# Performance work log

Measured on AMD Instinct MI355X. Metric: run time of the kernel, lower is better.

## Reference

```python
import jax, jax.numpy as jnp
import numpy as np

N = 20000      # nodes
E = 320000     # edges
IN = 300       # input_channel
HID = 100      # hidden_channel (= heads*out_channels with heads=1)
R = 50         # num_relations
B = 8          # num_bases (the 4th positional arg 'heads'=8 lands on num_bases in PyG RGATConv)
HEADS = 1
CLS = 3
Q = 64         # number of query (aspect) nodes
EPS = 1e-16


def setup_inputs() -> dict:
    key = jax.random.key(0)
    ks = jax.random.split(key, 16)
    x = jax.random.normal(ks[0], (N, IN), jnp.float32)
    edge_index = jax.random.randint(ks[1], (2, E), 0, N)
    edge_type = jax.random.randint(ks[2], (E,), 0, R)
    query_indices = jax.random.randint(ks[3], (Q,), 0, N)

    def w(k, shape, scale):
        return jax.random.normal(k, shape, jnp.float32) * scale

    comp1 = w(ks[4], (R, B), 0.3)
    basis1 = w(ks[5], (B, IN, HEADS * HID), 1.0 / np.sqrt(IN))
    q1 = w(ks[6], (HEADS * HID, HEADS), 0.1)
    k1 = w(ks[7], (HEADS * HID, HEADS), 0.1)
    b1 = jnp.zeros((HEADS * HID,), jnp.float32)
    comp2 = w(ks[8], (R, B), 0.3)
    basis2 = w(ks[9], (B, HID, HEADS * HID), 1.0 / np.sqrt(HID))
    q2 = w(ks[10], (HEADS * HID, HEADS), 0.1)
    k2 = w(ks[11], (HEADS * HID, HEADS), 0.1)
    b2 = jnp.zeros((HEADS * HID,), jnp.float32)
    Wl = w(ks[12], (CLS, HID), 1.0 / np.sqrt(HID))
    bl = jnp.zeros((CLS,), jnp.float32)
    return dict(x=x, edge_index=edge_index, edge_type=edge_type,
                query_indices=query_indices,
                comp1=comp1, basis1=basis1, q1=q1, k1=k1, b1=b1,
                comp2=comp2, basis2=basis2, q2=q2, k2=k2, b2=b2,
                Wl=Wl, bl=bl)


def segment_softmax(alpha, seg, num_segments):
    # numerically-stable softmax over edges grouped by destination node
    m = jax.ops.segment_max(alpha, seg, num_segments=num_segments)  # [N, H]
    e = jnp.exp(alpha - m[seg])
    s = jax.ops.segment_sum(e, seg, num_segments=num_segments)
    return e / (s[seg] + EPS)


def rgat_conv(x, edge_index, edge_type, comp, basis, q, k, b):
    # basis-decomposed per-relation weight: [R, in, H*out]
    W = jnp.einsum('rb,bio->rio', comp, basis)
    # transform every node under every relation once, then gather per edge
    xt = jnp.einsum('ni,rio->nro', x, W)          # [N, R, H*out]
    src, dst = edge_index[0], edge_index[1]        # j -> i (source_to_target)
    xi = xt[dst, edge_type]                        # [E, H*out]
    xj = xt[src, edge_type]                        # [E, H*out]
    qi = xi @ q                                    # [E, H]
    kj = xj @ k                                    # [E, H]
    alpha = jax.nn.leaky_relu(qi + kj, 0.2)        # additive self-attention
    alpha = segment_softmax(alpha, dst, N)         # across-relation softmax
    msg = xj.reshape(E, HEADS, HID) * alpha[:, :, None]
    out = jax.ops.segment_sum(msg, dst, num_segments=N)  # [N, H, out]
    return out.reshape(N, HEADS * HID) + b         # concat=True


def reference(x, edge_index, edge_type, query_indices,
              comp1, basis1, q1, k1, b1,
              comp2, basis2, q2, k2, b2, Wl, bl):
    h = jax.nn.relu(rgat_conv(x, edge_index, edge_type, comp1, basis1, q1, k1, b1))
    h = jax.nn.relu(rgat_conv(h, edge_index, edge_type, comp2, basis2, q2, k2, b2))
    pooled = h[query_indices].mean(axis=0)          # [HID]
    return pooled @ Wl.T + bl                       # [CLS]
```

## Files before the change

kernel.cpp:

```cpp
#include <hip/hip_runtime.h>
#include <math.h>

#define N_NODES 20000
#define E_EDGES 320000
#define IN_CH   300
#define HID     100
#define R_REL   50
#define NB      8
#define CLS     3
#define NQ      64
#define OUTW    800
#define ZW      128
#define KP1     320
#define KP2     128
#define SCAN_BLKS ((N_NODES + 255) / 256)

typedef unsigned short ushort_t;
typedef __attribute__((ext_vector_type(8))) short     short8;
typedef __attribute__((ext_vector_type(8))) unsigned short ushort8;
typedef __attribute__((ext_vector_type(4))) float     f32x4;
typedef __attribute__((ext_vector_type(2))) float     f32x2;

__device__ __forceinline__ ushort_t f2bf_rne(float f) {
    unsigned u = __float_as_uint(f);
    unsigned r = (u + 0x7fffu + ((u >> 16) & 1u)) >> 16;
    return (ushort_t)r;
}
__device__ __forceinline__ float bf2f(ushort_t u) {
    return __uint_as_float((unsigned)u << 16);
}

__global__ __launch_bounds__(256) void zero_deg2(int* __restrict__ dd,
                                                 int* __restrict__ ds) {
    int i = blockIdx.x * 256 + threadIdx.x;
    if (i < N_NODES) { dd[i] = 0; ds[i] = 0; }
}

__global__ __launch_bounds__(256) void hist2_kernel(
        const int* __restrict__ ei, int* __restrict__ dd,
        int* __restrict__ ds) {
    int e = blockIdx.x * 256 + threadIdx.x;
    if (e < E_EDGES) {
        atomicAdd(&dd[ei[E_EDGES + e]], 1);
        atomicAdd(&ds[ei[e]], 1);
    }
}

__global__ __launch_bounds__(256) void scan1_both(
        const int* __restrict__ deg_d, int* __restrict__ rp_d, int* __restrict__ bsum_d,
        const int* __restrict__ deg_s, int* __restrict__ rp_s, int* __restrict__ bsum_s) {
    int set = blockIdx.x / SCAN_BLKS, blk = blockIdx.x % SCAN_BLKS;
    const int* deg = set ? deg_s : deg_d;
    int* rowptr    = set ? rp_s  : rp_d;
    int* bsum      = set ? bsum_s : bsum_d;
    __shared__ int s[256];
    int tid = threadIdx.x;
    int idx = blk * 256 + tid;
    int v = (idx < N_NODES) ? deg[idx] : 0;
    s[tid] = v; __syncthreads();
    #pragma unroll
    for (int off = 1; off < 256; off <<= 1) {
        int t = (tid >= off) ? s[tid - off] : 0;
        __syncthreads();
        s[tid] += t;
        __syncthreads();
    }
    if (idx < N_NODES) rowptr[idx] = s[tid] - v;
    if (tid == 255) bsum[blk] = s[255];
}

__global__ __launch_bounds__(128) void scan2_both(
        int* __restrict__ bsum_d, int* __restrict__ rp_d,
        int* __restrict__ bsum_s, int* __restrict__ rp_s) {
    int* bsum   = blockIdx.x ? bsum_s : bsum_d;
    int* rowptr = blockIdx.x ? rp_s   : rp_d;
    __shared__ int s[128];
    int tid = threadIdx.x;
    int v = (tid < SCAN_BLKS) ? bsum[tid] : 0;
    s[tid] = v; __syncthreads();
    #pragma unroll
    for (int off = 1; off < 128; off <<= 1) {
        int t = (tid >= off) ? s[tid - off] : 0;
        __syncthreads();
        s[tid] += t;
        __syncthreads();
    }
    if (tid < SCAN_BLKS) bsum[tid] = s[tid] - v;
    if (tid == 0) rowptr[N_NODES] = E_EDGES;
}

__global__ __launch_bounds__(256) void scan3_both(
        int* __restrict__ rp_d, const int* __restrict__ bsum_d, int* __restrict__ cur_d,
        int* __restrict__ rp_s, const int* __restrict__ bsum_s, int* __restrict__ cur_s) {
    int set = blockIdx.x / SCAN_BLKS, blk = blockIdx.x % SCAN_BLKS;
    int* rowptr      = set ? rp_s   : rp_d;
    const int* bsum  = set ? bsum_s : bsum_d;
    int* cursor      = set ? cur_s  : cur_d;
    int idx = blk * 256 + threadIdx.x;
    if (idx < N_NODES) {
        int v = rowptr[idx] + bsum[blk];
        rowptr[idx] = v;
        cursor[idx] = v;
    }
}

__global__ __launch_bounds__(256) void scatter_both(
        const int* __restrict__ ei, const int* __restrict__ et,
        int* __restrict__ cur_d, int* __restrict__ cur_s,
        int* __restrict__ skey, int* __restrict__ skey_s,
        int* __restrict__ zidx) {
    int e = blockIdx.x * 256 + threadIdx.x;
    if (e >= E_EDGES) return;
    int s = ei[e], d = ei[E_EDGES + e], rt = et[e];
    int p = atomicAdd(&cur_d[d], 1);
    skey[p] = (s << 6) | rt;
    int qp = atomicAdd(&cur_s[s], 1);
    skey_s[qp] = rt;
    zidx[p] = qp;
}

__global__ __launch_bounds__(256) void split_bt_both(
        const float* __restrict__ basis1, ushort_t* __restrict__ Bt1,
        const float* __restrict__ basis2, ushort_t* __restrict__ Bt2) {
    int idx = blockIdx.x * 256 + threadIdx.x;
    const int n1 = OUTW * KP1;
    if (idx < n1) {
        int n = idx / KP1, k = idx - n * KP1;
        int b = n / HID, o = n - b * HID;
        float v = (k < IN_CH) ? basis1[((size_t)b * IN_CH + k) * HID + o] : 0.f;
        Bt1[idx] = f2bf_rne(v);
    } else {
        int i2 = idx - n1;
        if (i2 >= OUTW * KP2) return;
        int n = i2 / KP2, k = i2 - n * KP2;
        int b = n / HID, o = n - b * HID;
        float v = (k < HID) ? basis2[((size_t)b * HID + k) * HID + o] : 0.f;
        Bt2[i2] = f2bf_rne(v);
    }
}

#define BM 16
#define BN 160
#define NCB (OUTW / BN)
__global__ __launch_bounds__(128) void gemm_mfma(
        const float* __restrict__ A, const ushort_t* __restrict__ Bt,
        ushort_t* __restrict__ xbh, int M, int K, int Kp, int do_relu) {
    __shared__ ushort_t As[BM * 328];
    __shared__ ushort_t Bs[BN * 32];
    int tid  = threadIdx.x;
    int lane = tid & 63, wave = tid >> 6;
    int ml = lane & 15, quad = lane >> 4;
    int wc = wave * 80;
    int row0 = blockIdx.x * BM;
    int SW = Kp + 8;
    int ksteps = Kp >> 5;

    {
        int ra = tid >> 3;
        int gr = row0 + ra;
        const float* ar = A + (size_t)gr * K;
        for (int c = (tid & 7); c * 8 < Kp; c += 8) {
            int kb = c * 8;
            float vals[8];
            if (gr < M) {
                if (kb + 8 <= K) {
                    float4 f0 = *(const float4*)&ar[kb];
                    float4 f1 = *(const float4*)&ar[kb + 4];
                    vals[0]=f0.x; vals[1]=f0.y; vals[2]=f0.z; vals[3]=f0.w;
                    vals[4]=f1.x; vals[5]=f1.y; vals[6]=f1.z; vals[7]=f1.w;
                } else {
                    #pragma unroll
                    for (int i = 0; i < 8; i++)
                        vals[i] = (kb + i < K) ? ar[kb + i] : 0.f;
                }
                if (do_relu)
                    #pragma unroll
                    for (int i = 0; i < 8; i++) vals[i] = fmaxf(vals[i], 0.f);
            } else {
                #pragma unroll
                for (int i = 0; i < 8; i++) vals[i] = 0.f;
            }
            ushort8 hv;
            #pragma unroll
            for (int i = 0; i < 8; i++) hv[i] = f2bf_rne(vals[i]);
            *(ushort8*)&As[ra * SW + kb] = hv;
        }
    }

    for (int cb = 0; cb < NCB; cb++) {
        int col0 = cb * BN;
        f32x4 acc[5] = {};
        for (int ks = 0; ks < ksteps; ks++) {
            int k0 = ks << 5;
            __syncthreads();
            for (int t = tid; t < 640; t += 128) {
                int rb = t >> 2, ch = t & 3;
                __builtin_amdgcn_global_load_lds(
                    (const __attribute__((address_space(1))) unsigned int*)
                        &Bt[(size_t)(col0 + rb) * Kp + k0 + ch * 8],
                    (__attribute__((address_space(3))) unsigned int*)&Bs[t * 8],
                    16, 0, 0);
            }
            __syncthreads();
            short8 af, bf[5];
            af = *(const short8*)&As[ml * SW + k0 + quad * 8];
            #pragma unroll
            for (int nt = 0; nt < 5; nt++)
                bf[nt] = *(const short8*)&Bs[(wc + nt * 16 + ml) * 32 + quad * 8];
            #pragma unroll
            for (int nt = 0; nt < 5; nt++)
                acc[nt] = __builtin_amdgcn_mfma_f32_16x16x32_bf16(af, bf[nt], acc[nt], 0, 0, 0);
        }
        #pragma unroll
        for (int nt = 0; nt < 5; nt++) {
            #pragma unroll
            for (int r = 0; r < 4; r++) {
                int grow = row0 + quad * 4 + r;
                if (grow < M)
                    xbh[(size_t)grow * OUTW + col0 + wc + nt * 16 + ml] =
                        f2bf_rne(acc[nt][r]);
            }
        }
    }
}

__global__ __launch_bounds__(256) void qk3_kernel(
        const ushort_t* __restrict__ xbh, const float* __restrict__ q,
        const float* __restrict__ k, float* __restrict__ xbq,
        float* __restrict__ xbk) {
    __shared__ float sq[HID], sk[HID];
    int tid = threadIdx.x;
    if (tid < HID) { sq[tid] = q[tid]; sk[tid] = k[tid]; }
    __syncthreads();
    int idx = blockIdx.x * 256 + tid;
    if (idx >= N_NODES * NB) return;
    const ushort_t* xr = xbh + (size_t)(idx >> 3) * OUTW + (idx & 7) * HID;
    float aq = 0.f, ak = 0.f;
    #pragma unroll
    for (int c = 0; c < 25; c++) {
        ushort4 v = *(const ushort4*)&xr[c * 4];
        #pragma unroll
        for (int i = 0; i < 4; i++) {
            float f = bf2f(((const ushort_t*)&v)[i]);
            aq = fmaf(f, sq[c * 4 + i], aq);
            ak = fmaf(f, sk[c * 4 + i], ak);
        }
    }
    xbq[idx] = aq;
    xbk[idx] = ak;
}

__global__ __launch_bounds__(256) void compute_z(
        const int* __restrict__ rowptr_s, const int* __restrict__ skey_s,
        const float* __restrict__ comp, const ushort_t* __restrict__ xbh,
        ushort_t* __restrict__ Z) {
    __shared__ float scomp[R_REL * NB];
    int tid = threadIdx.x;
    for (int i = tid; i < R_REL * NB; i += 256) scomp[i] = comp[i];
    __syncthreads();
    int wave = tid >> 6, lane = tid & 63;
    int s = blockIdx.x * 4 + wave;
    if (s >= N_NODES) return;
    int beg = rowptr_s[s], end = rowptr_s[s + 1];
    if (beg == end) return;
    int eg = lane >> 4, c16 = lane & 15;
    int cbase = c16 * 8;
    float xr[NB][8];
    #pragma unroll
    for (int b = 0; b < NB; b++)
        #pragma unroll
        for (int i = 0; i < 8; i++) xr[b][i] = 0.f;
    if (cbase < HID) {
        #pragma unroll
        for (int b = 0; b < NB; b++) {
            const ushort_t* base = xbh + (size_t)s * OUTW + b * HID + cbase;
            ushort4 v0 = *(const ushort4*)base;
            xr[b][0] = bf2f(v0.x); xr[b][1] = bf2f(v0.y);
            xr[b][2] = bf2f(v0.z); xr[b][3] = bf2f(v0.w);
            if (cbase + 8 <= HID) {
                ushort4 v1 = *(const ushort4*)(base + 4);
                xr[b][4] = bf2f(v1.x); xr[b][5] = bf2f(v1.y);
                xr[b][6] = bf2f(v1.z); xr[b][7] = bf2f(v1.w);
            }
        }
    }
    for (int w0 = beg; w0 < end; w0 += 64) {
        int kw = (w0 + lane < end) ? skey_s[w0 + lane] : 0;
        int wend = w0 + 64 < end ? w0 + 64 : end;
        for (int p0 = w0; p0 < wend; p0 += 4) {
            int j = p0 - w0 + eg;
            int rt = __shfl(kw, j) & 63;
            int p = p0 + eg;
            const float* cr = &scomp[rt * NB];
            float z[8] = {};
            #pragma unroll
            for (int b = 0; b < NB; b++) {
                float cb = cr[b];
                #pragma unroll
                for (int i = 0; i < 8; i++) z[i] = fmaf(cb, xr[b][i], z[i]);
            }
            ushort8 zz;
            #pragma unroll
            for (int i = 0; i < 8; i++) zz[i] = f2bf_rne(z[i]);
            if (p < end)
                *(ushort8*)&Z[(size_t)p * ZW + cbase] = zz;
        }
    }
}

__global__ __launch_bounds__(256) void msg_soft(
        const int* __restrict__ rowptr, const int* __restrict__ skey,
        const int* __restrict__ zidx,
        const float* __restrict__ comp, const ushort_t* __restrict__ Z,
        const float* __restrict__ xbq, const float* __restrict__ xbk,
        const float* __restrict__ bias, float* __restrict__ h) {
    __shared__ float scomp[R_REL * NB];
    int tid = threadIdx.x;
    for (int i = tid; i < R_REL * NB; i += 256) scomp[i] = comp[i];
    __syncthreads();
    int wave = tid >> 6, lane = tid & 63;
    int d = blockIdx.x * 4 + wave;
    if (d >= N_NODES) return;
    int beg = rowptr[d], end = rowptr[d + 1];

    float4 qd0 = *(const float4*)&xbq[d * NB];
    float4 qd1 = *(const float4*)&xbq[d * NB + 4];

    int l5 = lane & 31;
    bool act = l5 < 25;
    int oc = l5 * 4;
    f32x4 acc = {0.f, 0.f, 0.f, 0.f};
    float m = -1e30f, l = 0.f;

    for (int c0 = beg; c0 < end; c0 += 64) {
        int p = c0 + lane;
        bool valid = p < end;
        float a = -1e30f;
        int zi = 0;
        if (valid) {
            int key = skey[p];
            zi = zidx[p];
            int s = key >> 6, rt = key & 63;
            const float4 c0v = *(const float4*)&scomp[rt * NB];
            const float4 c1v = *(const float4*)&scomp[rt * NB + 4];
            const float4 k0v = *(const float4*)&xbk[s * NB];
            const float4 k1v = *(const float4*)&xbk[s * NB + 4];
            float qi = c0v.x*qd0.x + c0v.y*qd0.y + c0v.z*qd0.z + c0v.w*qd0.w
                     + c1v.x*qd1.x + c1v.y*qd1.y + c1v.z*qd1.z + c1v.w*qd1.w;
            float kj = c0v.x*k0v.x + c0v.y*k0v.y + c0v.z*k0v.z + c0v.w*k0v.w
                     + c1v.x*k1v.x + c1v.y*k1v.y + c1v.z*k1v.z + c1v.w*k1v.w;
            a = qi + kj;
            a = a > 0.f ? a : 0.2f * a;
        }
        float cm = a;
        #pragma unroll
        for (int off = 32; off; off >>= 1) cm = fmaxf(cm, __shfl_xor(cm, off));
        float M = fmaxf(m, cm);
        float scale = __expf(m - M);
        acc *= scale; l *= scale; m = M;
        float wgt = valid ? __expf(a - M) : 0.f;
        float cs = wgt;
        #pragma unroll
        for (int off = 32; off; off >>= 1) cs += __shfl_xor(cs, off);
        l += cs;
        int cnt = end - c0; if (cnt > 64) cnt = 64;
        for (int j = 0; j < cnt; j += 2) {
            int jj = j + (lane >> 5);
            float wj = __shfl(wgt, jj);
            int   zj = __shfl(zi, jj);
            if (act) {
                ushort4 zz = *(const ushort4*)&Z[(size_t)zj * ZW + oc];
                acc.x = fmaf(wj, bf2f(zz.x), acc.x);
                acc.y = fmaf(wj, bf2f(zz.y), acc.y);
                acc.z = fmaf(wj, bf2f(zz.z), acc.z);
                acc.w = fmaf(wj, bf2f(zz.w), acc.w);
            }
        }
    }
    #pragma unroll
    for (int i = 0; i < 4; i++) acc[i] += __shfl_xor(acc[i], 32);
    if (lane < 25) {
        float inv = 1.f / (l + 1e-16f);
        float4 r;
        r.x = bias[oc]     + acc.x * inv;
        r.y = bias[oc + 1] + acc.y * inv;
        r.z = bias[oc + 2] + acc.z * inv;
        r.w = bias[oc + 3] + acc.w * inv;
        *(float4*)&h[(size_t)d * HID + oc] = r;
    }
}

__global__ __launch_bounds__(128) void head_kernel(
        const float* __restrict__ h2, const int* __restrict__ qidx,
        const float* __restrict__ Wl, const float* __restrict__ bl,
        float* __restrict__ out) {
    __shared__ float pooled[HID];
    int tid = threadIdx.x;
    if (tid < HID) {
        float s = 0.f;
        for (int i = 0; i < NQ; i++)
            s += fmaxf(h2[(size_t)qidx[i] * HID + tid], 0.f);
        pooled[tid] = s * (1.0f / NQ);
    }
    __syncthreads();
    if (tid < CLS) {
        float s = bl[tid];
        for (int o = 0; o < HID; o++) s = fmaf(pooled[o], Wl[tid * HID + o], s);
        out[tid] = s;
    }
}

extern "C" void kernel_launch(void* const* d_in, const int* in_sizes, int n_in,
                              void* d_out, int out_size, void* d_ws, size_t ws_size,
                              hipStream_t stream) {
    const float* x      = (const float*)d_in[0];
    const int*   ei     = (const int*)  d_in[1];
    const int*   et     = (const int*)  d_in[2];
    const int*   qidx   = (const int*)  d_in[3];
    const float* comp1  = (const float*)d_in[4];
    const float* basis1 = (const float*)d_in[5];
    const float* q1     = (const float*)d_in[6];
    const float* k1     = (const float*)d_in[7];
    const float* b1     = (const float*)d_in[8];
    const float* comp2  = (const float*)d_in[9];
    const float* basis2 = (const float*)d_in[10];
    const float* q2     = (const float*)d_in[11];
    const float* k2     = (const float*)d_in[12];
    const float* b2     = (const float*)d_in[13];
    const float* Wl     = (const float*)d_in[14];
    const float* bl     = (const float*)d_in[15];
    float* out = (float*)d_out;

    char* w = (char*)d_ws;
    size_t off = 0;
    auto alloc = [&](size_t nbytes) {
        void* p = (void*)(w + off);
        off += ((nbytes + 255) / 256) * 256;
        return p;
    };
    ushort_t* xbh    = (ushort_t*)alloc((size_t)N_NODES * OUTW * 2);
    ushort_t* Z      = (ushort_t*)alloc((size_t)E_EDGES * ZW * 2);
    float*    h1     = (float*)alloc((size_t)N_NODES * HID * 4);
    float*    h2     = (float*)alloc((size_t)N_NODES * HID * 4);
    ushort_t* Bt1    = (ushort_t*)alloc((size_t)OUTW * KP1 * 2);
    ushort_t* Bt2    = (ushort_t*)alloc((size_t)OUTW * KP2 * 2);
    float*    xbq    = (float*)alloc((size_t)N_NODES * NB * 4);
    float*    xbk    = (float*)alloc((size_t)N_NODES * NB * 4);
    int*      deg_d  = (int*)alloc(N_NODES * 4);
    int*      deg_s  = (int*)alloc(N_NODES * 4);
    int*      rp_d   = (int*)alloc((N_NODES + 1) * 4);
    int*      rp_s   = (int*)alloc((N_NODES + 1) * 4);
    int*      cur_d  = (int*)alloc(N_NODES * 4);
    int*      cur_s  = (int*)alloc(N_NODES * 4);
    int*      bsum_d = (int*)alloc(SCAN_BLKS * 4);
    int*      bsum_s = (int*)alloc(SCAN_BLKS * 4);
    int*      skey   = (int*)alloc(E_EDGES * 4);
    int*      skey_s = (int*)alloc(E_EDGES * 4);
    int*      zidx   = (int*)alloc(E_EDGES * 4);

    zero_deg2<<<SCAN_BLKS, 256, 0, stream>>>(deg_d, deg_s);
    hist2_kernel<<<(E_EDGES + 255) / 256, 256, 0, stream>>>(ei, deg_d, deg_s);
    scan1_both<<<2 * SCAN_BLKS, 256, 0, stream>>>(deg_d, rp_d, bsum_d, deg_s, rp_s, bsum_s);
    scan2_both<<<2, 128, 0, stream>>>(bsum_d, rp_d, bsum_s, rp_s);
    scan3_both<<<2 * SCAN_BLKS, 256, 0, stream>>>(rp_d, bsum_d, cur_d, rp_s, bsum_s, cur_s);
    scatter_both<<<(E_EDGES + 255) / 256, 256, 0, stream>>>(ei, et, cur_d, cur_s, skey, skey_s, zidx);
    split_bt_both<<<(OUTW * (KP1 + KP2) + 255) / 256, 256, 0, stream>>>(basis1, Bt1, basis2, Bt2);

    auto layer = [&](const float* input, int K, int Kp, int relu_in,
                     const ushort_t* Bt, const float* comp, const float* q,
                     const float* k, const float* bias, float* hout) {
        gemm_mfma<<<(N_NODES + BM - 1) / BM, 128, 0, stream>>>(input, Bt, xbh, N_NODES, K, Kp, relu_in);
        qk3_kernel<<<(N_NODES * NB + 255) / 256, 256, 0, stream>>>(xbh, q, k, xbq, xbk);
        compute_z<<<(N_NODES + 3) / 4, 256, 0, stream>>>(rp_s, skey_s, comp, xbh, Z);
        msg_soft<<<(N_NODES + 3) / 4, 256, 0, stream>>>(rp_d, skey, zidx, comp, Z, xbq, xbk, bias, hout);
    };

    layer(x,  IN_CH, KP1, 0, Bt1, comp1, q1, k1, b1, h1);
    layer(h1, HID,   KP2, 1, Bt2, comp2, q2, k2, b2, h2);
    head_kernel<<<1, 128, 0, stream>>>(h2, qidx, Wl, bl, out);
}
```

Measured before the change: 369.5 us.

## Restructure basis GEMM to register-held A fragments and direct global B loads

The basis GEMM is rewritten so each wave keeps its entire row of A as bf16 MFMA fragments in registers, and B fragments are read straight from global/L2 instead of being staged through LDS with per-k-step barriers. Blocks grow to 512 threads covering 64 rows by 160 columns per pass, and K and the ReLU flag become template parameters so the k-loop fully unrolls. This removes the LDS staging and the __syncthreads in the inner loop. In exchange it costs more registers (up to 10 A fragments), and each wave now fetches its B fragments from global/L2 on its own, since there is no cross-wave sharing through LDS.

```diff
diff --git a/kernel.cpp b/kernel.cpp
--- a/kernel.cpp
+++ b/kernel.cpp
@@ -139,77 +139,62 @@
     }
 }
 
-#define BM 16
-#define BN 160
-#define NCB (OUTW / BN)
-__global__ __launch_bounds__(128) void gemm_mfma(
+template<int K, int RELU>
+__global__ __launch_bounds__(512, 4) void gemm_mfma(
         const float* __restrict__ A, const ushort_t* __restrict__ Bt,
-        ushort_t* __restrict__ xbh, int M, int K, int Kp, int do_relu) {
-    __shared__ ushort_t As[BM * 328];
-    __shared__ ushort_t Bs[BN * 32];
+        ushort_t* __restrict__ xbh, int M) {
+    constexpr int KSTEPS = (K + 31) / 32;
+    constexpr int KP = KSTEPS * 32;
     int tid  = threadIdx.x;
     int lane = tid & 63, wave = tid >> 6;
+    int wr = wave >> 1, wc = wave & 1;
     int ml = lane & 15, quad = lane >> 4;
-    int wc = wave * 80;
-    int row0 = blockIdx.x * BM;
-    int SW = Kp + 8;
-    int ksteps = Kp >> 5;
-
+    int row0 = blockIdx.x * 64 + wr * 16;
+
+    short8 afrag[KSTEPS];
     {
-        int ra = tid >> 3;
-        int gr = row0 + ra;
+        int gr = row0 + ml;
+        bool rowok = gr < M;
         const float* ar = A + (size_t)gr * K;
-        for (int c = (tid & 7); c * 8 < Kp; c += 8) {
-            int kb = c * 8;
-            float vals[8];
-            if (gr < M) {
-                if (kb + 8 <= K) {
-                    float4 f0 = *(const float4*)&ar[kb];
-                    float4 f1 = *(const float4*)&ar[kb + 4];
-                    vals[0]=f0.x; vals[1]=f0.y; vals[2]=f0.z; vals[3]=f0.w;
-                    vals[4]=f1.x; vals[5]=f1.y; vals[6]=f1.z; vals[7]=f1.w;
-                } else {
-                    #pragma unroll
-                    for (int i = 0; i < 8; i++)
-                        vals[i] = (kb + i < K) ? ar[kb + i] : 0.f;
-                }
-                if (do_relu)
-                    #pragma unroll
-                    for (int i = 0; i < 8; i++) vals[i] = fmaxf(vals[i], 0.f);
+        #pragma unroll
+        for (int ks = 0; ks < KSTEPS; ks++) {
+            int kb = ks * 32 + quad * 8;
+            float v[8];
+            if (rowok && kb + 8 <= K) {
+                float4 f0 = *(const float4*)&ar[kb];
+                float4 f1 = *(const float4*)&ar[kb + 4];
+                v[0]=f0.x; v[1]=f0.y; v[2]=f0.z; v[3]=f0.w;
+                v[4]=f1.x; v[5]=f1.y; v[6]=f1.z; v[7]=f1.w;
             } else {
                 #pragma unroll
-                for (int i = 0; i < 8; i++) vals[i] = 0.f;
-            }
-            ushort8 hv;
-            #pragma unroll
-            for (int i = 0; i < 8; i++) hv[i] = f2bf_rne(vals[i]);
-            *(ushort8*)&As[ra * SW + kb] = hv;
-        }
-    }
-
-    for (int cb = 0; cb < NCB; cb++) {
-        int col0 = cb * BN;
+                for (int i = 0; i < 8; i++)
+                    v[i] = (rowok && kb + i < K) ? ar[kb + i] : 0.f;
+            }
+            if (RELU) {
+                #pragma unroll
+                for (int i = 0; i < 8; i++) v[i] = fmaxf(v[i], 0.f);
+            }
+            short8 hv;
+            #pragma unroll
+            for (int i = 0; i < 8; i++) hv[i] = (short)f2bf_rne(v[i]);
+            afrag[ks] = hv;
+        }
+    }
+
+    for (int cb = 0; cb < 5; cb++) {
+        int col0 = cb * 160 + wc * 80;
+        const ushort_t* bp0 = Bt + (size_t)(col0 + ml) * KP + quad * 8;
         f32x4 acc[5] = {};
-        for (int ks = 0; ks < ksteps; ks++) {
-            int k0 = ks << 5;
-            __syncthreads();
-            for (int t = tid; t < 640; t += 128) {
-                int rb = t >> 2, ch = t & 3;
-                __builtin_amdgcn_global_load_lds(
-                    (const __attribute__((address_space(1))) unsigned int*)
-                        &Bt[(size_t)(col0 + rb) * Kp + k0 + ch * 8],
-                    (__attribute__((address_space(3))) unsigned int*)&Bs[t * 8],
-                    16, 0, 0);
-            }
-            __syncthreads();
-            short8 af, bf[5];
-            af = *(const short8*)&As[ml * SW + k0 + quad * 8];
+        #pragma unroll
+        for (int ks = 0; ks < KSTEPS; ks++) {
+            short8 bf[5];
             #pragma unroll
             for (int nt = 0; nt < 5; nt++)
-                bf[nt] = *(const short8*)&Bs[(wc + nt * 16 + ml) * 32 + quad * 8];
+                bf[nt] = *(const short8*)(bp0 + (size_t)nt * 16 * KP + ks * 32);
             #pragma unroll
             for (int nt = 0; nt < 5; nt++)
-                acc[nt] = __builtin_amdgcn_mfma_f32_16x16x32_bf16(af, bf[nt], acc[nt], 0, 0, 0);
+                acc[nt] = __builtin_amdgcn_mfma_f32_16x16x32_bf16(
+                              afrag[ks], bf[nt], acc[nt], 0, 0, 0);
         }
         #pragma unroll
         for (int nt = 0; nt < 5; nt++) {
@@ -217,7 +202,7 @@
             for (int r = 0; r < 4; r++) {
                 int grow = row0 + quad * 4 + r;
                 if (grow < M)
-                    xbh[(size_t)grow * OUTW + col0 + wc + nt * 16 + ml] =
+                    xbh[(size_t)grow * OUTW + col0 + nt * 16 + ml] =
                         f2bf_rne(acc[nt][r]);
             }
         }
@@ -466,16 +451,17 @@
     scatter_both<<<(E_EDGES + 255) / 256, 256, 0, stream>>>(ei, et, cur_d, cur_s, skey, skey_s, zidx);
     split_bt_both<<<(OUTW * (KP1 + KP2) + 255) / 256, 256, 0, stream>>>(basis1, Bt1, basis2, Bt2);
 
-    auto layer = [&](const float* input, int K, int Kp, int relu_in,
-                     const ushort_t* Bt, const float* comp, const float* q,
-                     const float* k, const float* bias, float* hout) {
-        gemm_mfma<<<(N_NODES + BM - 1) / BM, 128, 0, stream>>>(input, Bt, xbh, N_NODES, K, Kp, relu_in);
-        qk3_kernel<<<(N_NODES * NB + 255) / 256, 256, 0, stream>>>(xbh, q, k, xbq, xbk);
-        compute_z<<<(N_NODES + 3) / 4, 256, 0, stream>>>(rp_s, skey_s, comp, xbh, Z);
-        msg_soft<<<(N_NODES + 3) / 4, 256, 0, stream>>>(rp_d, skey, zidx, comp, Z, xbq, xbk, bias, hout);
-    };
-
-    layer(x,  IN_CH, KP1, 0, Bt1, comp1, q1, k1, b1, h1);
-    layer(h1, HID,   KP2, 1, Bt2, comp2, q2, k2, b2, h2);
+    const int GGRID = (N_NODES + 63) / 64;
+
+    gemm_mfma<IN_CH, 0><<<GGRID, 512, 0, stream>>>(x, Bt1, xbh, N_NODES);
+    qk3_kernel<<<(N_NODES * NB + 255) / 256, 256, 0, stream>>>(xbh, q1, k1, xbq, xbk);
+    compute_z<<<(N_NODES + 3) / 4, 256, 0, stream>>>(rp_s, skey_s, comp1, xbh, Z);
+    msg_soft<<<(N_NODES + 3) / 4, 256, 0, stream>>>(rp_d, skey, zidx, comp1, Z, xbq, xbk, b1, h1);
+
+    gemm_mfma<HID, 1><<<GGRID, 512, 0, stream>>>(h1, Bt2, xbh, N_NODES);
+    qk3_kernel<<<(N_NODES * NB + 255) / 256, 256, 0, stream>>>(xbh, q2, k2, xbq, xbk);
+    compute_z<<<(N_NODES + 3) / 4, 256, 0, stream>>>(rp_s, skey_s, comp2, xbh, Z);
+    msg_soft<<<(N_NODES + 3) / 4, 256, 0, stream>>>(rp_d, skey, zidx, comp2, Z, xbq, xbk, b2, h2);
+
     head_kernel<<<1, 128, 0, stream>>>(h2, qidx, Wl, bl, out);
 }
```

New measurement: 478.5 us. 29.5% more time.
